# Kernel tuning notes

Hardware: AMD Instinct MI355X
Metric: run time of the kernel (lower is better)

Reference implementation:

```python
import jax, jax.numpy as jnp
import numpy as np

EPS = 1e-6

def _rms_norm(x, w):
    # torch: x / (||x||_2 * n^{-1/2} + eps) * w
    rms = jnp.linalg.norm(x, axis=-1, keepdims=True) * (x.shape[-1] ** -0.5)
    return x / (rms + EPS) * w

def _rope_cos_sin(seq_len, head_dim):
    half = head_dim // 2
    freq = 1.0 / (10000.0 ** (jnp.arange(half, dtype=jnp.float32) / half))
    t = jnp.arange(seq_len, dtype=jnp.float32)
    freqs = t[:, None] * freq[None, :]            # [s, half]
    freqs = jnp.concatenate([freqs, freqs], -1)   # [s, d_head]
    cos = jnp.cos(freqs)[None, :, None, :]        # [1, s, 1, d_head]
    sin = jnp.sin(freqs)[None, :, None, :]
    return cos, sin

def _rotate_half(x):
    h = x.shape[-1] // 2
    return jnp.concatenate([-x[..., h:], x[..., :h]], -1)

def setup_inputs() -> dict:
    key = jax.random.key(0)
    ks = jax.random.split(key, 8)
    B, S, D, H, F = 2, 2048, 2048, 16, 128
    return {
        'query_input': jax.random.normal(ks[0], (B, S, D), jnp.float32),
        'key_input':   jax.random.normal(ks[1], (B, S, D), jnp.float32),
        'value_input': jax.random.normal(ks[2], (B, S, D), jnp.float32),
        'W_Q': jax.random.normal(ks[3], (H, D, F), jnp.float32) * (D ** -0.5),
        'W_K': jax.random.normal(ks[4], (H, D, F), jnp.float32) * (D ** -0.5),
        'W_V': jax.random.normal(ks[5], (H, D, F), jnp.float32) * (D ** -0.5),
        'W_O': jax.random.normal(ks[6], (H, F, D), jnp.float32) * (F ** -0.5),
        'b_Q': jnp.zeros((H, F), jnp.float32),
        'b_K': jnp.zeros((H, F), jnp.float32),
        'b_V': jnp.zeros((H, F), jnp.float32),
        'b_O': jnp.zeros((D,), jnp.float32),
        'q_norm_w': jnp.ones((F,), jnp.float32),
        'k_norm_w': jnp.ones((F,), jnp.float32),
    }

def reference(query_input, key_input, value_input, W_Q, W_K, W_V, W_O,
              b_Q, b_K, b_V, b_O, q_norm_w, k_norm_w):
    head_dim = W_Q.shape[-1]
    q = jnp.einsum('bpd,hdf->bphf', query_input, W_Q) + b_Q[None, None]
    k = jnp.einsum('bpd,hdf->bphf', key_input,   W_K) + b_K[None, None]
    v = jnp.einsum('bpd,hdf->bphf', value_input, W_V) + b_V[None, None]
    q = _rms_norm(q, q_norm_w)
    k = _rms_norm(k, k_norm_w)
    cos, sin = _rope_cos_sin(q.shape[1], head_dim)
    q = q * cos + _rotate_half(q) * sin
    k = k * cos + _rotate_half(k) * sin
    scores = jnp.einsum('bphf,bqhf->bhpq', q, k) / (head_dim ** 0.5)
    pattern = jax.nn.softmax(scores, axis=-1)
    attn = jnp.einsum('bhpq,bqhf->bphf', pattern, v)
    return jnp.einsum('bphf,hfm->bpm', attn, W_O) + b_O
```

## Files before the change

kernel.cpp:

```cpp
#include <hip/hip_runtime.h>
#include <stdint.h>

typedef unsigned short u16;
typedef __attribute__((ext_vector_type(8))) short  s8b;
typedef __attribute__((ext_vector_type(4))) float  f32x4;

#define S_LEN   2048
#define NHEAD   16
#define HD      128
#define DM      2048
#define NB      2
#define NPLANE  (NB*NHEAD)
#define ROWS    (NB*S_LEN)
#define PLANE_ELEMS (S_LEN*HD)
#define ATT_SCALE 0.08838834764831845f
#define LOG2E     1.4426950408889634f

__device__ __forceinline__ float bf2f(u16 u){
  union { unsigned u; float f; } x; x.u = ((unsigned)u) << 16; return x.f;
}
__device__ __forceinline__ u16 f2bf(float f){
  union { float f; unsigned u; } x; x.f = f;
  unsigned r = x.u + 0x7FFFu + ((x.u >> 16) & 1u);
  return (u16)(r >> 16);
}
__device__ __forceinline__ unsigned cvtpk(float lo, float hi){
  unsigned r;
  asm("v_cvt_pk_bf16_f32 %0, %1, %2" : "=v"(r) : "v"(lo), "v"(hi));
  return r;
}

typedef const __attribute__((address_space(1))) unsigned int* gas1;
typedef __attribute__((address_space(3))) unsigned int* las3;
__device__ __forceinline__ void gload16(const void* g, void* l){
  __builtin_amdgcn_global_load_lds((gas1)g, (las3)l, 16, 0, 0);
}

__device__ __forceinline__ f32x4 mfma16(s8b a, s8b b, f32x4 c){
  return __builtin_amdgcn_mfma_f32_16x16x32_bf16(a, b, c, 0, 0, 0);
}

__global__ __launch_bounds__(256) void cvt4x3(const float4* __restrict__ a,
                                              const float4* __restrict__ b,
                                              const float4* __restrict__ c,
                                              uint2* __restrict__ oa,
                                              uint2* __restrict__ ob,
                                              uint2* __restrict__ oc, int n4){
  int i = blockIdx.x*256 + threadIdx.x;
  if (i >= n4) return;
  const float4* src = (blockIdx.y == 0) ? a : (blockIdx.y == 1) ? b : c;
  uint2*       dst  = (blockIdx.y == 0) ? oa : (blockIdx.y == 1) ? ob : oc;
  float4 v = src[i];
  uint2 o;
  o.x = (unsigned)f2bf(v.x) | ((unsigned)f2bf(v.y) << 16);
  o.y = (unsigned)f2bf(v.z) | ((unsigned)f2bf(v.w) << 16);
  dst[i] = o;
}

__global__ __launch_bounds__(256) void transpose_cvt(const float* __restrict__ in,
                                                     u16* __restrict__ out,
                                                     int R, int C, int outStride){
  __shared__ float tile[32][33];
  int z = blockIdx.z;
  const float* inz = in + (size_t)z * R * C;
  u16* outz = out + (size_t)z * C * outStride;
  int r0 = blockIdx.x*32, c0 = blockIdx.y*32;
  int tx = threadIdx.x, ty = threadIdx.y;
  #pragma unroll
  for (int i=0;i<4;i++)
    tile[ty*4+i][tx] = inz[(size_t)(r0+ty*4+i)*C + c0 + tx];
  __syncthreads();
  #pragma unroll
  for (int i=0;i<4;i++)
    outz[(size_t)(c0+ty*4+i)*outStride + r0 + tx] = f2bf(tile[tx][ty*4+i]);
}

__global__ __launch_bounds__(256) void rope_tab(float* __restrict__ ctab,
                                                float* __restrict__ stab){
  int i = blockIdx.x*256 + threadIdx.x;
  int p = i >> 6, j = i & 63;
  float freq = exp2f(-(float)j * (13.287712379549449f/64.0f));
  float a = (float)p * freq;
  ctab[i] = cosf(a);
  stab[i] = sinf(a);
}

__global__ __launch_bounds__(512) void gemm_bt(const u16* __restrict__ A,
                                               const u16* __restrict__ BT,
                                               const float* __restrict__ bias,
                                               void* __restrict__ out, int mode){
  const int K = 2048;
  const int NT = 32;
  __shared__ u16 lds[6*12288];
  const int t = threadIdx.x, w = t >> 6, l = t & 63;
  const int lr = l & 15, lg = l >> 4;
  const int wr = w >> 1, wc = w & 1;
  int bid = blockIdx.x;
  int swz = (bid & 7)*32 + (bid >> 3);
  const int M0 = (swz >> 4) * 256, N0 = (swz & 15) * 128;

  f32x4 acc[4][4];
  #pragma unroll
  for (int i=0;i<4;i++)
    #pragma unroll
    for (int j=0;j<4;j++) acc[i][j] = f32x4{0.f,0.f,0.f,0.f};

  auto stageH = [&](int ttu, int h){
    int slot = (2*ttu + h) % 6;
    int tt   = ttu & 31;
    char* base = (char*)&lds[slot*12288];
    #pragma unroll
    for (int j=0;j<2;j++){
      int d = w*2048 + j*1024 + l*16;
      int row = d >> 7;
      int koff = ((l&7)*16) ^ ((row&7)<<4);
      gload16((const char*)A + ((size_t)(M0 + h*128 + row)*K + tt*64)*2 + koff,
              base + w*2048 + j*1024);
    }
    {
      int d = w*1024 + l*16;
      int row = d >> 7;
      int koff = ((l&7)*16) ^ ((row&7)<<4);
      gload16((const char*)BT + ((size_t)(N0 + h*64 + row)*K + tt*64)*2 + koff,
              base + 16384 + w*1024);
    }
  };

  stageH(0,0); stageH(0,1); stageH(1,0); stageH(1,1);

  for (int kt=0; kt<NT; kt++){
    const char* Ab = (const char*)&lds[((2*kt + (wr>>1)) % 6)*12288];
    const char* Bb = (const char*)&lds[((2*kt + wc) % 6)*12288] + 16384;

    stageH(kt+2, 0);
    asm volatile("s_waitcnt vmcnt(9)" ::: "memory");
    __builtin_amdgcn_s_barrier();
    __builtin_amdgcn_sched_barrier(0);

    s8b af[4][2];
    #pragma unroll
    for (int mi=0;mi<4;mi++)
      #pragma unroll
      for (int kc=0;kc<2;kc++){
        int rA = (wr&1)*64 + mi*16 + lr;
        af[mi][kc] = *(const s8b*)(Ab + rA*128 + ((kc*64 + lg*16) ^ ((rA&7)<<4)));
      }
    {
      s8b bf[2][2];
      #pragma unroll
      for (int nj=0;nj<2;nj++){
        int rB = nj*16 + lr;
        bf[nj][0] = *(const s8b*)(Bb + rB*128 + ((0*64 + lg*16) ^ ((rB&7)<<4)));
        bf[nj][1] = *(const s8b*)(Bb + rB*128 + ((1*64 + lg*16) ^ ((rB&7)<<4)));
      }
      __builtin_amdgcn_s_setprio(1);
      #pragma unroll
      for (int mi=0;mi<4;mi++)
        #pragma unroll
        for (int nj=0;nj<2;nj++){
          acc[mi][nj] = mfma16(af[mi][0], bf[nj][0], acc[mi][nj]);
          acc[mi][nj] = mfma16(af[mi][1], bf[nj][1], acc[mi][nj]);
        }
      __builtin_amdgcn_s_setprio(0);
    }
    stageH(kt+2, 1);
    {
      s8b bf[2][2];
      #pragma unroll
      for (int nj=0;nj<2;nj++){
        int rB = (nj+2)*16 + lr;
        bf[nj][0] = *(const s8b*)(Bb + rB*128 + ((0*64 + lg*16) ^ ((rB&7)<<4)));
        bf[nj][1] = *(const s8b*)(Bb + rB*128 + ((1*64 + lg*16) ^ ((rB&7)<<4)));
      }
      __builtin_amdgcn_s_setprio(1);
      #pragma unroll
      for (int mi=0;mi<4;mi++)
        #pragma unroll
        for (int nj=0;nj<2;nj++){
          acc[mi][nj+2] = mfma16(af[mi][0], bf[nj][0], acc[mi][nj+2]);
          acc[mi][nj+2] = mfma16(af[mi][1], bf[nj][1], acc[mi][nj+2]);
        }
      __builtin_amdgcn_s_setprio(0);
    }
    __builtin_amdgcn_sched_barrier(0);
    __builtin_amdgcn_s_barrier();
    __builtin_amdgcn_sched_barrier(0);
  }
  asm volatile("s_waitcnt vmcnt(0)" ::: "memory");

  #pragma unroll
  for (int mi=0;mi<4;mi++){
    int growb = M0 + wr*64 + mi*16 + lg*4;
    #pragma unroll
    for (int nj=0;nj<4;nj++){
      int gcol = N0 + wc*64 + nj*16 + lr;
      float bv = bias[gcol];
      #pragma unroll
      for (int r=0;r<4;r++){
        int grow = growb + r;
        float v = acc[mi][nj][r] + bv;
        if (mode == 2){
          ((float*)out)[(size_t)grow*2048 + gcol] = v;
        } else {
          int b = grow >> 11, p = grow & 2047;
          int h = gcol >> 7,  f = gcol & 127;
          if (mode == 0){
            ((u16*)out)[(((size_t)(b*NHEAD+h))*S_LEN + p)*HD + f] = f2bf(v);
          } else {
            size_t base = ((size_t)(b*NHEAD+h)*PLANE_ELEMS)*2 + (size_t)(p>>6)*16384;
            int p6 = p & 63;
            int q_ = ((p6&12)<<1) | (p6&3) | ((p6&16)>>2);
            int kvp = (p6 & 32) | q_;
            int kc = kvp >> 5, lgv = (kvp >> 3) & 3, jv = kvp & 7;
            int off = (kc*8 + (f>>4))*1024 + (lgv*16 + (f&15))*16 + jv*2;
            *(u16*)((char*)out + base + off) = f2bf(v);
          }
        }
      }
    }
  }
}

__global__ __launch_bounds__(256) void norm_rope(const u16* __restrict__ in,
                                                 u16* __restrict__ outp,
                                                 const float* __restrict__ nw,
                                                 const float* __restrict__ ctab,
                                                 const float* __restrict__ stab,
                                                 int swizzled, float oscale){
  int t = threadIdx.x, w = t>>6, l = t&63;
  size_t R = (size_t)blockIdx.x*4 + w;
  int p = (int)(R & (S_LEN-1));
  size_t base = R * HD;
  float x0 = bf2f(in[base + l]);
  float x1 = bf2f(in[base + 64 + l]);
  float ss = x0*x0 + x1*x1;
  #pragma unroll
  for (int m=1;m<64;m<<=1) ss += __shfl_xor(ss, m);
  float rms = sqrtf(ss * (1.0f/128.0f));
  float sc = oscale / (rms + 1e-6f);
  float xn0 = x0 * sc * nw[l];
  float xn1 = x1 * sc * nw[64+l];
  float c = ctab[(size_t)p*64 + l], s = stab[(size_t)p*64 + l];
  float o0 = xn0*c - xn1*s;
  float o1 = xn1*c + xn0*s;
  if (!swizzled){
    outp[base + l]      = f2bf(o0);
    outp[base + 64 + l] = f2bf(o1);
  } else {
    size_t plane = R >> 11;
    int kv = p & 63;
    size_t tb = (plane*(size_t)PLANE_ELEMS + (size_t)(p>>6)*8192) * 2;
    int b0 = (kv*256 + l*2)        ^ ((kv&7)<<4);
    int b1 = (kv*256 + (64+l)*2)   ^ ((kv&7)<<4);
    *(u16*)((char*)outp + tb + b0) = f2bf(o0);
    *(u16*)((char*)outp + tb + b1) = f2bf(o1);
  }
}

__global__ __launch_bounds__(256,2) void attn_fwd(const u16* __restrict__ qn,
                                                  const u16* __restrict__ kn,
                                                  const u16* __restrict__ vt,
                                                  u16* __restrict__ attn_out){
  __shared__ u16 Klds[2][8192];
  int t = threadIdx.x, w = t>>6, l = t&63;
  int lr = l&15, lg = l>>4;

  int bid = blockIdx.x;
  int xcd = bid & 7, j = bid >> 3;
  int plane = xcd*4 + (j >> 4);
  int qb = j & 15;
  int q0 = qb*128 + w*32;

  const s8b ones = { (short)0x3F80, (short)0x3F80, (short)0x3F80, (short)0x3F80,
                     (short)0x3F80, (short)0x3F80, (short)0x3F80, (short)0x3F80 };

  s8b qf[2][4];
  #pragma unroll
  for (int qi=0; qi<2; qi++)
    #pragma unroll
    for (int fc=0; fc<4; fc++)
      qf[qi][fc] = *(const s8b*)(qn + ((size_t)plane*S_LEN + q0 + qi*16 + lr)*HD + fc*32 + lg*8);

  f32x4 lacc[2];
  lacc[0] = f32x4{0.f,0.f,0.f,0.f};
  lacc[1] = f32x4{0.f,0.f,0.f,0.f};
  f32x4 oacc[2][8];
  #pragma unroll
  for (int qi=0;qi<2;qi++)
    #pragma unroll
    for (int i=0;i<8;i++) oacc[qi][i] = f32x4{0.f,0.f,0.f,0.f};

  const u16* kbase = kn + (size_t)plane*PLANE_ELEMS;
  const char* vbase = (const char*)vt + (size_t)plane*PLANE_ELEMS*2;

  auto stage = [&](int buf, int kt){
    #pragma unroll
    for (int i=0;i<4;i++)
      gload16(kbase + (size_t)kt*8192 + w*2048 + i*512 + l*8, &Klds[buf][w*2048 + i*512]);
  };

  stage(0, 0);
  int cur = 0;
  for (int kt=0; kt<32; kt++){
    __syncthreads();
    if (kt+1 < 32) stage(cur^1, kt+1);

    const char* vb = vbase + (size_t)kt*16384;
    s8b vf0[8];
    #pragma unroll
    for (int fc2=0; fc2<8; fc2++)
      vf0[fc2] = *(const s8b*)(vb + fc2*1024 + l*16);

    f32x4 sacc[4][2];
    #pragma unroll
    for (int c=0;c<4;c++){
      sacc[c][0] = f32x4{0.f,0.f,0.f,0.f};
      sacc[c][1] = f32x4{0.f,0.f,0.f,0.f};
    }
    __builtin_amdgcn_s_setprio(1);
    #pragma unroll
    for (int c=0;c<4;c++){
      int kv = c*16 + lr;
      #pragma unroll
      for (int fc=0; fc<4; fc++){
        int byte = (kv*256 + (fc*32 + lg*8)*2) ^ ((kv&7)<<4);
        s8b kf = *(const s8b*)((const char*)&Klds[cur][0] + byte);
        sacc[c][0] = mfma16(kf, qf[0][fc], sacc[c][0]);
        sacc[c][1] = mfma16(kf, qf[1][fc], sacc[c][1]);
      }
    }
    __builtin_amdgcn_s_setprio(0);

    s8b vf1[8];
    #pragma unroll
    for (int fc2=0; fc2<8; fc2++)
      vf1[fc2] = *(const s8b*)(vb + (8+fc2)*1024 + l*16);

    float pv[2][4][4];
    #pragma unroll
    for (int qi=0;qi<2;qi++)
      #pragma unroll
      for (int c=0;c<4;c++){
        pv[qi][c][0] = exp2f(sacc[c][qi][0]);
        pv[qi][c][1] = exp2f(sacc[c][qi][1]);
        pv[qi][c][2] = exp2f(sacc[c][qi][2]);
        pv[qi][c][3] = exp2f(sacc[c][qi][3]);
      }

    s8b pa[2][2];
    #pragma unroll
    for (int qi=0;qi<2;qi++)
      #pragma unroll
      for (int kc=0;kc<2;kc++){
        union { s8b v; unsigned u[4]; } pu;
        pu.u[0] = cvtpk(pv[qi][2*kc][0],   pv[qi][2*kc][1]);
        pu.u[1] = cvtpk(pv[qi][2*kc][2],   pv[qi][2*kc][3]);
        pu.u[2] = cvtpk(pv[qi][2*kc+1][0], pv[qi][2*kc+1][1]);
        pu.u[3] = cvtpk(pv[qi][2*kc+1][2], pv[qi][2*kc+1][3]);
        pa[qi][kc] = pu.v;
      }

    __builtin_amdgcn_s_setprio(1);
    lacc[0] = mfma16(pa[0][0], ones, lacc[0]);
    lacc[1] = mfma16(pa[1][0], ones, lacc[1]);
    #pragma unroll
    for (int fc2=0; fc2<8; fc2++){
      oacc[0][fc2] = mfma16(pa[0][0], vf0[fc2], oacc[0][fc2]);
      oacc[1][fc2] = mfma16(pa[1][0], vf0[fc2], oacc[1][fc2]);
    }
    lacc[0] = mfma16(pa[0][1], ones, lacc[0]);
    lacc[1] = mfma16(pa[1][1], ones, lacc[1]);
    #pragma unroll
    for (int fc2=0; fc2<8; fc2++){
      oacc[0][fc2] = mfma16(pa[0][1], vf1[fc2], oacc[0][fc2]);
      oacc[1][fc2] = mfma16(pa[1][1], vf1[fc2], oacc[1][fc2]);
    }
    __builtin_amdgcn_s_setprio(0);
    cur ^= 1;
  }

  int b = plane >> 4, h = plane & 15;
  #pragma unroll
  for (int qi=0;qi<2;qi++){
    float inv[4];
    #pragma unroll
    for (int r=0;r<4;r++) inv[r] = 1.0f / lacc[qi][r];
    #pragma unroll
    for (int fc2=0; fc2<8; fc2++){
      int f = fc2*16 + lr;
      #pragma unroll
      for (int r=0;r<4;r++){
        int row = q0 + qi*16 + lg*4 + r;
        float o = oacc[qi][fc2][r] * inv[r];
        attn_out[(((size_t)b*S_LEN + row)*NHEAD + h)*HD + f] = f2bf(o);
      }
    }
  }
}

extern "C" void kernel_launch(void* const* d_in, const int* in_sizes, int n_in,
                              void* d_out, int out_size, void* d_ws, size_t ws_size,
                              hipStream_t stream){
  const float* xq = (const float*)d_in[0];
  const float* xk = (const float*)d_in[1];
  const float* xv = (const float*)d_in[2];
  const float* WQ = (const float*)d_in[3];
  const float* WK = (const float*)d_in[4];
  const float* WV = (const float*)d_in[5];
  const float* WO = (const float*)d_in[6];
  const float* bQ = (const float*)d_in[7];
  const float* bK = (const float*)d_in[8];
  const float* bV = (const float*)d_in[9];
  const float* bO = (const float*)d_in[10];
  const float* qw = (const float*)d_in[11];
  const float* kw = (const float*)d_in[12];

  char* ws = (char*)d_ws;
  size_t off = 0;
  auto alloc = [&](size_t bytes)->void*{
    void* p = ws + off; off += (bytes + 255) & ~(size_t)255; return p;
  };
  const size_t ACT = (size_t)ROWS*DM*2;
  const size_t WMT = (size_t)DM*DM*2;
  u16* xqb  = (u16*)alloc(ACT);
  u16* xkb  = (u16*)alloc(ACT);
  u16* xvb  = (u16*)alloc(ACT);
  u16* WqT  = (u16*)alloc(WMT);
  u16* WkT  = (u16*)alloc(WMT);
  u16* WvT  = (u16*)alloc(WMT);
  u16* WoT  = (u16*)alloc(WMT);
  u16* qraw = (u16*)alloc(ACT);
  u16* kraw = (u16*)alloc(ACT);
  u16* knT  = (u16*)alloc(ACT);
  u16* vtS  = (u16*)alloc(ACT);
  u16* attn = (u16*)alloc(ACT);
  float* ctab = (float*)alloc((size_t)S_LEN*64*4);
  float* stab = (float*)alloc((size_t)S_LEN*64*4);
  if (off > ws_size) return;

  const int n4 = ROWS*DM/4;
  cvt4x3<<<dim3(n4/256, 3), dim3(256), 0, stream>>>((const float4*)xq, (const float4*)xk,
                                                    (const float4*)xv, (uint2*)xqb,
                                                    (uint2*)xkb, (uint2*)xvb, n4);
  rope_tab<<<dim3(S_LEN*64/256), dim3(256), 0, stream>>>(ctab, stab);
  transpose_cvt<<<dim3(64,4,16), dim3(32,8), 0, stream>>>(WQ, WqT, 2048, 128, 2048);
  transpose_cvt<<<dim3(64,4,16), dim3(32,8), 0, stream>>>(WK, WkT, 2048, 128, 2048);
  transpose_cvt<<<dim3(64,4,16), dim3(32,8), 0, stream>>>(WV, WvT, 2048, 128, 2048);
  transpose_cvt<<<dim3(64,64,1), dim3(32,8), 0, stream>>>(WO, WoT, 2048, 2048, 2048);

  gemm_bt<<<dim3(256), dim3(512), 0, stream>>>(xqb, WqT, bQ, qraw, 0);
  gemm_bt<<<dim3(256), dim3(512), 0, stream>>>(xkb, WkT, bK, kraw, 0);
  gemm_bt<<<dim3(256), dim3(512), 0, stream>>>(xvb, WvT, bV, vtS, 1);

  norm_rope<<<dim3(NPLANE*S_LEN/4), dim3(256), 0, stream>>>(qraw, qraw, qw, ctab, stab, 0, ATT_SCALE*LOG2E);
  norm_rope<<<dim3(NPLANE*S_LEN/4), dim3(256), 0, stream>>>(kraw, knT, kw, ctab, stab, 1, 1.0f);

  attn_fwd<<<dim3(512), dim3(256), 0, stream>>>(qraw, knT, vtS, attn);

  gemm_bt<<<dim3(256), dim3(512), 0, stream>>>(attn, WoT, bO, d_out, 2);
}
```

Baseline: 342.6 us.

## Merge Q/K norm-rope launches and deepen attention K staging to four buffers

Merges the two norm_rope launches into one, with blockIdx.y choosing the Q or K path, which removes one kernel launch. In attention, K tiles now rotate through four LDS buffers. Two tiles are prefetched and processed per barrier, which halves the number of __syncthreads and gives loads more time to land. LDS use per block doubles to 64KB, which may limit how many blocks fit on each CU alongside the launch bound of 2.

New measurement: 334.3 us. -2.4%, faster.

```diff
diff --git a/kernel.cpp b/kernel.cpp
--- a/kernel.cpp
+++ b/kernel.cpp
@@ -221,13 +221,21 @@
   }
 }
 
-__global__ __launch_bounds__(256) void norm_rope(const u16* __restrict__ in,
-                                                 u16* __restrict__ outp,
-                                                 const float* __restrict__ nw,
-                                                 const float* __restrict__ ctab,
-                                                 const float* __restrict__ stab,
-                                                 int swizzled, float oscale){
+__global__ __launch_bounds__(256) void norm_rope2(const u16* __restrict__ qin,
+                                                  u16* __restrict__ qout,
+                                                  const float* __restrict__ qwv,
+                                                  const u16* __restrict__ kin,
+                                                  u16* __restrict__ kout,
+                                                  const float* __restrict__ kwv,
+                                                  const float* __restrict__ ctab,
+                                                  const float* __restrict__ stab,
+                                                  float qscale){
   int t = threadIdx.x, w = t>>6, l = t&63;
+  int isK = blockIdx.y;
+  const u16* in  = isK ? kin  : qin;
+  u16*       outp= isK ? kout : qout;
+  const float* nw= isK ? kwv  : qwv;
+  float oscale   = isK ? 1.0f : qscale;
   size_t R = (size_t)blockIdx.x*4 + w;
   int p = (int)(R & (S_LEN-1));
   size_t base = R * HD;
@@ -243,7 +251,7 @@
   float c = ctab[(size_t)p*64 + l], s = stab[(size_t)p*64 + l];
   float o0 = xn0*c - xn1*s;
   float o1 = xn1*c + xn0*s;
-  if (!swizzled){
+  if (!isK){
     outp[base + l]      = f2bf(o0);
     outp[base + 64 + l] = f2bf(o1);
   } else {
@@ -261,7 +269,7 @@
                                                   const u16* __restrict__ kn,
                                                   const u16* __restrict__ vt,
                                                   u16* __restrict__ attn_out){
-  __shared__ u16 Klds[2][8192];
+  __shared__ u16 Klds[4][8192];
   int t = threadIdx.x, w = t>>6, l = t&63;
   int lr = l&15, lg = l>>4;
 
@@ -299,12 +307,7 @@
       gload16(kbase + (size_t)kt*8192 + w*2048 + i*512 + l*8, &Klds[buf][w*2048 + i*512]);
   };
 
-  stage(0, 0);
-  int cur = 0;
-  for (int kt=0; kt<32; kt++){
-    __syncthreads();
-    if (kt+1 < 32) stage(cur^1, kt+1);
-
+  auto tile = [&](int buf, int kt){
     const char* vb = vbase + (size_t)kt*16384;
     s8b vf0[8];
     #pragma unroll
@@ -324,7 +327,7 @@
       #pragma unroll
       for (int fc=0; fc<4; fc++){
         int byte = (kv*256 + (fc*32 + lg*8)*2) ^ ((kv&7)<<4);
-        s8b kf = *(const s8b*)((const char*)&Klds[cur][0] + byte);
+        s8b kf = *(const s8b*)((const char*)&Klds[buf][0] + byte);
         sacc[c][0] = mfma16(kf, qf[0][fc], sacc[c][0]);
         sacc[c][1] = mfma16(kf, qf[1][fc], sacc[c][1]);
       }
@@ -376,7 +379,18 @@
       oacc[1][fc2] = mfma16(pa[1][1], vf1[fc2], oacc[1][fc2]);
     }
     __builtin_amdgcn_s_setprio(0);
-    cur ^= 1;
+  };
+
+  stage(0, 0); stage(1, 1);
+  for (int it=0; it<16; it++){
+    __syncthreads();
+    int b0 = (2*it) & 3, b1 = (2*it+1) & 3;
+    if (it < 15){
+      stage((2*it+2)&3, 2*it+2);
+      stage((2*it+3)&3, 2*it+3);
+    }
+    tile(b0, 2*it);
+    tile(b1, 2*it+1);
   }
 
   int b = plane >> 4, h = plane & 15;
@@ -452,8 +466,9 @@
   gemm_bt<<<dim3(256), dim3(512), 0, stream>>>(xkb, WkT, bK, kraw, 0);
   gemm_bt<<<dim3(256), dim3(512), 0, stream>>>(xvb, WvT, bV, vtS, 1);
 
-  norm_rope<<<dim3(NPLANE*S_LEN/4), dim3(256), 0, stream>>>(qraw, qraw, qw, ctab, stab, 0, ATT_SCALE*LOG2E);
-  norm_rope<<<dim3(NPLANE*S_LEN/4), dim3(256), 0, stream>>>(kraw, knT, kw, ctab, stab, 1, 1.0f);
+  norm_rope2<<<dim3(NPLANE*S_LEN/4, 2), dim3(256), 0, stream>>>(qraw, qraw, qw,
+                                                                kraw, knT, kw,
+                                                                ctab, stab, ATT_SCALE*LOG2E);
 
   attn_fwd<<<dim3(512), dim3(256), 0, stream>>>(qraw, knT, vtS, attn);
 
```
